# Optimization experiments

Hardware: AMD Instinct MI355X
Metric: run time of the kernel (lower is better)

The kernel has to match this reference:

```python
import jax, jax.numpy as jnp
import numpy as np
from jax import lax

BN_EPS = 1e-5

def dwconv(x, w, dilation):
    # x: [N,C,H,W], w: [C,1,k,k] depthwise; SAME padding = (r*(k-1)+1)//2
    k = w.shape[-1]
    pad = (dilation * (k - 1) + 1) // 2
    return lax.conv_general_dilated(
        x, w, window_strides=(1, 1), padding=[(pad, pad), (pad, pad)],
        rhs_dilation=(dilation, dilation), feature_group_count=x.shape[1],
        dimension_numbers=('NCHW', 'OIHW', 'NCHW'))

def bn_eval(y, gamma, beta, mean, var):
    # inference BatchNorm2d over channel dim; params: [C]
    inv = gamma * lax.rsqrt(var + BN_EPS)
    return y * inv[None, :, None, None] + (beta - mean * inv)[None, :, None, None]

def setup_inputs() -> dict:
    key = jax.random.key(0)
    ks = jax.random.split(key, 13)
    C = 384
    x = jax.random.normal(ks[0], (16, C, 56, 56), jnp.float32)
    w_lk = jax.random.normal(ks[1], (C, 1, 13, 13), jnp.float32) * 0.05
    w_b0 = jax.random.normal(ks[2], (C, 1, 5, 5), jnp.float32) * 0.05
    w_b1 = jax.random.normal(ks[3], (C, 1, 7, 7), jnp.float32) * 0.05
    w_b2 = jax.random.normal(ks[4], (C, 1, 7, 7), jnp.float32) * 0.05
    w_b3 = jax.random.normal(ks[5], (C, 1, 3, 3), jnp.float32) * 0.05
    w_b4 = jax.random.normal(ks[6], (C, 1, 3, 3), jnp.float32) * 0.05
    w_b5 = jax.random.normal(ks[7], (C, 1, 3, 3), jnp.float32) * 0.05
    bn_gamma = jax.random.uniform(ks[8], (7, C), jnp.float32, 0.5, 1.5)
    bn_beta = jax.random.normal(ks[9], (7, C), jnp.float32) * 0.1
    bn_mean = jax.random.normal(ks[10], (7, C), jnp.float32) * 0.1
    bn_var = jax.random.uniform(ks[11], (7, C), jnp.float32, 0.5, 1.5)
    return dict(x=x, w_lk=w_lk, w_b0=w_b0, w_b1=w_b1, w_b2=w_b2, w_b3=w_b3,
                w_b4=w_b4, w_b5=w_b5, bn_gamma=bn_gamma, bn_beta=bn_beta,
                bn_mean=bn_mean, bn_var=bn_var)

def reference(x, w_lk, w_b0, w_b1, w_b2, w_b3, w_b4, w_b5,
              bn_gamma, bn_beta, bn_mean, bn_var):
    # DilatedReparamBlock (kernel_size=13, non-deploy):
    # out = BN(dw13(x)) + sum_i BN_i(dw_{k_i, r_i}(x))
    dilates = (1, 1, 2, 3, 4, 5)
    branch_ws = (w_b0, w_b1, w_b2, w_b3, w_b4, w_b5)
    out = bn_eval(dwconv(x, w_lk, 1), bn_gamma[0], bn_beta[0], bn_mean[0], bn_var[0])
    for i, (w, r) in enumerate(zip(branch_ws, dilates)):
        j = i + 1
        out = out + bn_eval(dwconv(x, w, r), bn_gamma[j], bn_beta[j], bn_mean[j], bn_var[j])
    return out
```

## Files before the change

kernel.cpp:

```cpp
#include <hip/hip_runtime.h>


#define CCH 384
#define SP 56
#define PW 68
#define NPLANES (16*384)

__global__ __launch_bounds__(64, 2) void drb_conv13_r8(
    const float* __restrict__ x,
    const float* __restrict__ w_lk, const float* __restrict__ w_b0,
    const float* __restrict__ w_b1, const float* __restrict__ w_b2,
    const float* __restrict__ w_b3, const float* __restrict__ w_b4,
    const float* __restrict__ w_b5,
    const float* __restrict__ gamma, const float* __restrict__ beta,
    const float* __restrict__ mean, const float* __restrict__ var,
    float* __restrict__ out)
{
    __shared__ __align__(16) float sx[PW * PW];
    __shared__ __align__(16) float sw[13 * 16];

    const int plane = blockIdx.x;
    const int c = plane % CCH;
    const int tid = threadIdx.x;
    const float* __restrict__ xp = x + (size_t)plane * (SP * SP);

    float4 stage[13];
    #pragma unroll
    for (int k = 0; k < 13; k++) {
        int i4 = tid + 64 * k;
        if (i4 < SP * SP / 4) stage[k] = ((const float4*)xp)[i4];
    }

    float S[7];
    float bias = 0.f;
    #pragma unroll
    for (int j = 0; j < 7; j++) {
        float inv = gamma[j * CCH + c] * rsqrtf(var[j * CCH + c] + 1e-5f);
        S[j] = inv;
        bias += beta[j * CCH + c] - mean[j * CCH + c] * inv;
    }

    {
        float4 z = make_float4(0.f, 0.f, 0.f, 0.f);
        #pragma unroll
        for (int k = 0; k < 19; k++) {
            int i = tid + 64 * k;
            if (i < PW * PW / 4) ((float4*)sx)[i] = z;
        }
    }

    #pragma unroll
    for (int k = 0; k < 4; k++) {
        int t = tid + 64 * k;
        if (t < 13 * 16) {
            int ky = t >> 4, kx = t & 15;
            float w = 0.f;
            if (kx < 13) {
                w = S[0] * w_lk[c * 169 + ky * 13 + kx];
                if (ky >= 4 && ky <= 8 && kx >= 4 && kx <= 8)
                    w += S[1] * w_b0[c * 25 + (ky - 4) * 5 + (kx - 4)];
                if (ky >= 3 && ky <= 9 && kx >= 3 && kx <= 9)
                    w += S[2] * w_b1[c * 49 + (ky - 3) * 7 + (kx - 3)];
                if (!(ky & 1) && !(kx & 1))
                    w += S[3] * w_b2[c * 49 + (ky >> 1) * 7 + (kx >> 1)];
                if (ky >= 3 && ky <= 9 && (ky - 3) % 3 == 0 &&
                    kx >= 3 && kx <= 9 && (kx - 3) % 3 == 0)
                    w += S[4] * w_b3[c * 9 + ((ky - 3) / 3) * 3 + (kx - 3) / 3];
                if (ky >= 2 && ky <= 10 && (ky - 2) % 4 == 0 &&
                    kx >= 2 && kx <= 10 && (kx - 2) % 4 == 0)
                    w += S[5] * w_b4[c * 9 + ((ky - 2) / 4) * 3 + (kx - 2) / 4];
                if (ky >= 1 && ky <= 11 && (ky - 1) % 5 == 0 &&
                    kx >= 1 && kx <= 11 && (kx - 1) % 5 == 0)
                    w += S[6] * w_b5[c * 9 + ((ky - 1) / 5) * 3 + (kx - 1) / 5];
            }
            sw[t] = w;
        }
    }

    #pragma unroll
    for (int k = 0; k < 13; k++) {
        int i4 = tid + 64 * k;
        if (i4 < SP * SP / 4) {
            int r = i4 / 14;
            int col = (i4 - r * 14) * 4;
            float* d = &sx[(r + 6) * PW + col + 6];
            ((float2*)d)[0] = make_float2(stage[k].x, stage[k].y);
            ((float2*)d)[1] = make_float2(stage[k].z, stage[k].w);
        }
    }
    __syncthreads();

    const int xg = tid & 7;
    const int yg = tid >> 3;
    const int xgc = (xg < 7) ? xg : 3;
    const int Yb = yg * 7;
    const float* __restrict__ sbase = &sx[Yb * PW + 8 * xgc];

    float acc[7][8];
    #pragma unroll
    for (int r = 0; r < 7; r++)
        #pragma unroll
        for (int j = 0; j < 8; j++) acc[r][j] = 0.f;

    {
        float wA[7][13];
        #pragma unroll
        for (int dy = 0; dy < 7; dy++) {
            const float* wr = &sw[dy * 16];
            #pragma unroll
            for (int q = 0; q < 3; q++) {
                float4 t = ((const float4*)wr)[q];
                wA[dy][4*q+0] = t.x; wA[dy][4*q+1] = t.y;
                wA[dy][4*q+2] = t.z; wA[dy][4*q+3] = t.w;
            }
            wA[dy][12] = wr[12];
        }
        #pragma unroll
        for (int i = 0; i < 13; i++) {
            float4 win4[5];
            #pragma unroll
            for (int q = 0; q < 5; q++)
                win4[q] = *(const float4*)(sbase + i * PW + 4 * q);
            const float* win = (const float*)win4;
            #pragma unroll
            for (int dy = 0; dy < 7; dy++) {
                const int r = i - dy;
                if (r >= 0 && r < 7) {
                    #pragma unroll
                    for (int kx = 0; kx < 13; kx++) {
                        const float wv = wA[dy][kx];
                        #pragma unroll
                        for (int j = 0; j < 8; j++)
                            acc[r][j] = fmaf(wv, win[kx + j], acc[r][j]);
                    }
                }
            }
        }
    }

    {
        float wB[6][13];
        #pragma unroll
        for (int dy = 0; dy < 6; dy++) {
            const float* wr = &sw[(7 + dy) * 16];
            #pragma unroll
            for (int q = 0; q < 3; q++) {
                float4 t = ((const float4*)wr)[q];
                wB[dy][4*q+0] = t.x; wB[dy][4*q+1] = t.y;
                wB[dy][4*q+2] = t.z; wB[dy][4*q+3] = t.w;
            }
            wB[dy][12] = wr[12];
        }
        #pragma unroll
        for (int i = 7; i < 19; i++) {
            float4 win4[5];
            #pragma unroll
            for (int q = 0; q < 5; q++)
                win4[q] = *(const float4*)(sbase + i * PW + 4 * q);
            const float* win = (const float*)win4;
            #pragma unroll
            for (int dy = 0; dy < 6; dy++) {
                const int r = i - 7 - dy;
                if (r >= 0 && r < 7) {
                    #pragma unroll
                    for (int kx = 0; kx < 13; kx++) {
                        const float wv = wB[dy][kx];
                        #pragma unroll
                        for (int j = 0; j < 8; j++)
                            acc[r][j] = fmaf(wv, win[kx + j], acc[r][j]);
                    }
                }
            }
        }
    }

    if (xg < 7) {
        float* op = out + (size_t)plane * (SP * SP) + Yb * SP + 8 * xg;
        #pragma unroll
        for (int r = 0; r < 7; r++) {
            float4 v0 = make_float4(acc[r][0] + bias, acc[r][1] + bias,
                                    acc[r][2] + bias, acc[r][3] + bias);
            float4 v1 = make_float4(acc[r][4] + bias, acc[r][5] + bias,
                                    acc[r][6] + bias, acc[r][7] + bias);
            *(float4*)(op + r * SP) = v0;
            *(float4*)(op + r * SP + 4) = v1;
        }
    }
}

extern "C" void kernel_launch(void* const* d_in, const int* in_sizes, int n_in,
                              void* d_out, int out_size, void* d_ws, size_t ws_size,
                              hipStream_t stream) {
    const float* x    = (const float*)d_in[0];
    const float* w_lk = (const float*)d_in[1];
    const float* w_b0 = (const float*)d_in[2];
    const float* w_b1 = (const float*)d_in[3];
    const float* w_b2 = (const float*)d_in[4];
    const float* w_b3 = (const float*)d_in[5];
    const float* w_b4 = (const float*)d_in[6];
    const float* w_b5 = (const float*)d_in[7];
    const float* bn_g = (const float*)d_in[8];
    const float* bn_b = (const float*)d_in[9];
    const float* bn_m = (const float*)d_in[10];
    const float* bn_v = (const float*)d_in[11];
    float* out = (float*)d_out;

    drb_conv13_r8<<<dim3(NPLANES), dim3(64), 0, stream>>>(
        x, w_lk, w_b0, w_b1, w_b2, w_b3, w_b4, w_b5,
        bn_g, bn_b, bn_m, bn_v, out);
}
```

Measured before the change: 269.8 us.

## Move most conv weights to scalar registers and zero only the shared-memory halo

Most of the 13x13 folded weight rows are passed through readfirstlane so the compiler can keep them in scalar registers instead of per-lane vector registers. Fewer VGPRs are needed, and the launch-bounds occupancy hint is dropped. The padded input tile is no longer zeroed in full; only the halo border rows and columns are cleared, which cuts LDS stores before the barrier. The risk is that scalar-operand limits on VALU FMAs force extra moves, or that changed register allocation lowers occupancy.

```diff
diff --git a/kernel.cpp b/kernel.cpp
--- a/kernel.cpp
+++ b/kernel.cpp
@@ -6,7 +6,11 @@
 #define PW 68
 #define NPLANES (16*384)
 
-__global__ __launch_bounds__(64, 2) void drb_conv13_r8(
+__device__ __forceinline__ float rfl(float v) {
+    return __int_as_float(__builtin_amdgcn_readfirstlane(__float_as_int(v)));
+}
+
+__global__ __launch_bounds__(64) void drb_conv13_r11(
     const float* __restrict__ x,
     const float* __restrict__ w_lk, const float* __restrict__ w_b0,
     const float* __restrict__ w_b1, const float* __restrict__ w_b2,
@@ -41,11 +45,24 @@
     }
 
     {
-        float4 z = make_float4(0.f, 0.f, 0.f, 0.f);
-        #pragma unroll
-        for (int k = 0; k < 19; k++) {
-            int i = tid + 64 * k;
-            if (i < PW * PW / 4) ((float4*)sx)[i] = z;
+        float4 z4 = make_float4(0.f, 0.f, 0.f, 0.f);
+        float2 z2 = make_float2(0.f, 0.f);
+        #pragma unroll
+        for (int k = 0; k < 4; k++) {
+            int task = tid + 64 * k;
+            if (task < 204) {
+                int rr = task / 17;
+                int c4 = task - rr * 17;
+                int row = (rr < 6) ? rr : (rr + 56);
+                ((float4*)&sx[row * PW])[c4] = z4;
+            }
+        }
+        if (tid < 56) {
+            float* rp = &sx[(6 + tid) * PW];
+            *(float4*)(rp) = z4;
+            *(float2*)(rp + 4) = z2;
+            *(float2*)(rp + 62) = z2;
+            *(float4*)(rp + 64) = z4;
         }
     }
 
@@ -103,17 +120,29 @@
         for (int j = 0; j < 8; j++) acc[r][j] = 0.f;
 
     {
-        float wA[7][13];
-        #pragma unroll
-        for (int dy = 0; dy < 7; dy++) {
+        float wS[5][13];
+        float wV[2][13];
+        #pragma unroll
+        for (int dy = 0; dy < 5; dy++) {
             const float* wr = &sw[dy * 16];
             #pragma unroll
             for (int q = 0; q < 3; q++) {
                 float4 t = ((const float4*)wr)[q];
-                wA[dy][4*q+0] = t.x; wA[dy][4*q+1] = t.y;
-                wA[dy][4*q+2] = t.z; wA[dy][4*q+3] = t.w;
-            }
-            wA[dy][12] = wr[12];
+                wS[dy][4*q+0] = rfl(t.x); wS[dy][4*q+1] = rfl(t.y);
+                wS[dy][4*q+2] = rfl(t.z); wS[dy][4*q+3] = rfl(t.w);
+            }
+            wS[dy][12] = rfl(wr[12]);
+        }
+        #pragma unroll
+        for (int dy = 0; dy < 2; dy++) {
+            const float* wr = &sw[(5 + dy) * 16];
+            #pragma unroll
+            for (int q = 0; q < 3; q++) {
+                float4 t = ((const float4*)wr)[q];
+                wV[dy][4*q+0] = t.x; wV[dy][4*q+1] = t.y;
+                wV[dy][4*q+2] = t.z; wV[dy][4*q+3] = t.w;
+            }
+            wV[dy][12] = wr[12];
         }
         #pragma unroll
         for (int i = 0; i < 13; i++) {
@@ -123,12 +152,25 @@
                 win4[q] = *(const float4*)(sbase + i * PW + 4 * q);
             const float* win = (const float*)win4;
             #pragma unroll
-            for (int dy = 0; dy < 7; dy++) {
+            for (int dy = 0; dy < 5; dy++) {
                 const int r = i - dy;
                 if (r >= 0 && r < 7) {
                     #pragma unroll
                     for (int kx = 0; kx < 13; kx++) {
-                        const float wv = wA[dy][kx];
+                        const float wv = wS[dy][kx];
+                        #pragma unroll
+                        for (int j = 0; j < 8; j++)
+                            acc[r][j] = fmaf(wv, win[kx + j], acc[r][j]);
+                    }
+                }
+            }
+            #pragma unroll
+            for (int dy = 5; dy < 7; dy++) {
+                const int r = i - dy;
+                if (r >= 0 && r < 7) {
+                    #pragma unroll
+                    for (int kx = 0; kx < 13; kx++) {
+                        const float wv = wV[dy - 5][kx];
                         #pragma unroll
                         for (int j = 0; j < 8; j++)
                             acc[r][j] = fmaf(wv, win[kx + j], acc[r][j]);
@@ -139,17 +181,28 @@
     }
 
     {
-        float wB[6][13];
-        #pragma unroll
-        for (int dy = 0; dy < 6; dy++) {
+        float wS[5][13];
+        float wV[1][13];
+        #pragma unroll
+        for (int dy = 0; dy < 5; dy++) {
             const float* wr = &sw[(7 + dy) * 16];
             #pragma unroll
             for (int q = 0; q < 3; q++) {
                 float4 t = ((const float4*)wr)[q];
-                wB[dy][4*q+0] = t.x; wB[dy][4*q+1] = t.y;
-                wB[dy][4*q+2] = t.z; wB[dy][4*q+3] = t.w;
-            }
-            wB[dy][12] = wr[12];
+                wS[dy][4*q+0] = rfl(t.x); wS[dy][4*q+1] = rfl(t.y);
+                wS[dy][4*q+2] = rfl(t.z); wS[dy][4*q+3] = rfl(t.w);
+            }
+            wS[dy][12] = rfl(wr[12]);
+        }
+        {
+            const float* wr = &sw[12 * 16];
+            #pragma unroll
+            for (int q = 0; q < 3; q++) {
+                float4 t = ((const float4*)wr)[q];
+                wV[0][4*q+0] = t.x; wV[0][4*q+1] = t.y;
+                wV[0][4*q+2] = t.z; wV[0][4*q+3] = t.w;
+            }
+            wV[0][12] = wr[12];
         }
         #pragma unroll
         for (int i = 7; i < 19; i++) {
@@ -159,12 +212,24 @@
                 win4[q] = *(const float4*)(sbase + i * PW + 4 * q);
             const float* win = (const float*)win4;
             #pragma unroll
-            for (int dy = 0; dy < 6; dy++) {
+            for (int dy = 0; dy < 5; dy++) {
                 const int r = i - 7 - dy;
                 if (r >= 0 && r < 7) {
                     #pragma unroll
                     for (int kx = 0; kx < 13; kx++) {
-                        const float wv = wB[dy][kx];
+                        const float wv = wS[dy][kx];
+                        #pragma unroll
+                        for (int j = 0; j < 8; j++)
+                            acc[r][j] = fmaf(wv, win[kx + j], acc[r][j]);
+                    }
+                }
+            }
+            {
+                const int r = i - 12;
+                if (r >= 0 && r < 7) {
+                    #pragma unroll
+                    for (int kx = 0; kx < 13; kx++) {
+                        const float wv = wV[0][kx];
                         #pragma unroll
                         for (int j = 0; j < 8; j++)
                             acc[r][j] = fmaf(wv, win[kx + j], acc[r][j]);
@@ -205,7 +270,7 @@
     const float* bn_v = (const float*)d_in[11];
     float* out = (float*)d_out;
 
-    drb_conv13_r8<<<dim3(NPLANES), dim3(64), 0, stream>>>(
+    drb_conv13_r11<<<dim3(NPLANES), dim3(64), 0, stream>>>(
         x, w_lk, w_b0, w_b1, w_b2, w_b3, w_b4, w_b5,
         bn_g, bn_b, bn_m, bn_v, out);
 }
```

Result: no change. 269.4 us (-0.1%).
